# Kernel optimization log

Hardware: AMD Instinct MI355X
Metric: run time of the kernel (lower is better)

Reference implementation:

```python
import jax, jax.numpy as jnp
import numpy as np

WS = (5, 8, 8)   # window_size (Wz, Wh, Ww)
SS = (2, 4, 4)   # shift_size  (Sz, Sh, Sw)
EPS = 1e-5


def _rel_pos_index(ws):
    Wz, Wh, Ww = ws
    coords = np.stack(np.meshgrid(np.arange(Wz), np.arange(Wh), np.arange(Ww), indexing='ij'))
    cf = coords.reshape(3, -1)                      # (3, N)
    rel = cf[:, :, None] - cf[:, None, :]           # (3, N, N)
    rel = rel.transpose(1, 2, 0).astype(np.int64)   # (N, N, 3)
    rel[..., 0] += Wz - 1
    rel[..., 1] += Wh - 1
    rel[..., 2] += Ww - 1
    rel[..., 0] *= (2 * Wh - 1) * (2 * Ww - 1)
    rel[..., 1] *= (2 * Ww - 1)
    return rel.sum(-1)                              # (N, N)


def _shift_mask(Z, H, W, ws, ss):
    Wz, Wh, Ww = ws
    Sz, Sh, Sw = ss
    img = np.zeros((Z, H, W), dtype=np.float32)
    cnt = 0
    for zs in (slice(0, -Wz), slice(-Wz, -Sz), slice(-Sz, None)):
        for hs in (slice(0, -Wh), slice(-Wh, -Sh), slice(-Sh, None)):
            for wl in (slice(0, -Ww), slice(-Ww, -Sw), slice(-Sw, None)):
                img[zs, hs, wl] = cnt
                cnt += 1
    mw = img.reshape(Z // Wz, Wz, H // Wh, Wh, W // Ww, Ww)
    mw = mw.transpose(0, 2, 4, 1, 3, 5).reshape(-1, Wz * Wh * Ww)  # (nW, N)
    diff = mw[:, None, :] - mw[:, :, None]                          # (nW, N, N)
    return np.where(diff != 0, np.float32(-100.0), np.float32(0.0))


def _layernorm(x, g, b):
    mu = jnp.mean(x, axis=-1, keepdims=True)
    var = jnp.var(x, axis=-1, keepdims=True)
    return (x - mu) * jax.lax.rsqrt(var + EPS) * g + b


def setup_inputs() -> dict:
    key = jax.random.key(0)
    ks = jax.random.split(key, 6)
    B, C, Z, H, W = 2, 192, 10, 48, 48
    nH = 6
    hidden = 4 * C
    tbl = (2 * WS[0] - 1) * (2 * WS[1] - 1) * (2 * WS[2] - 1)
    return {
        'x': jax.random.normal(ks[0], (B, C, Z, H, W), jnp.float32),
        'norm1_g': jnp.ones((C,), jnp.float32),
        'norm1_b': jnp.zeros((C,), jnp.float32),
        'qkv_w': jax.random.normal(ks[1], (3 * C, C), jnp.float32) * 0.02,
        'qkv_b': jnp.zeros((3 * C,), jnp.float32),
        'proj_w': jax.random.normal(ks[2], (C, C), jnp.float32) * 0.02,
        'proj_b': jnp.zeros((C,), jnp.float32),
        'rpb_table': jax.random.normal(ks[3], (tbl, nH), jnp.float32) * 0.02,
        'norm2_g': jnp.ones((C,), jnp.float32),
        'norm2_b': jnp.zeros((C,), jnp.float32),
        'fc1_w': jax.random.normal(ks[4], (hidden, C), jnp.float32) * 0.02,
        'fc1_b': jnp.zeros((hidden,), jnp.float32),
        'fc2_w': jax.random.normal(ks[5], (C, hidden), jnp.float32) * 0.02,
        'fc2_b': jnp.zeros((C,), jnp.float32),
    }


def reference(x, norm1_g, norm1_b, qkv_w, qkv_b, proj_w, proj_b, rpb_table,
              norm2_g, norm2_b, fc1_w, fc1_b, fc2_w, fc2_b):
    B, C, Z, H, W = x.shape
    Wz, Wh, Ww = WS
    Sz, Sh, Sw = SS
    nH = rpb_table.shape[1]
    hd = C // nH
    N = Wz * Wh * Ww
    scale = hd ** -0.5

    h = jnp.transpose(x, (0, 2, 3, 4, 1))            # (B,Z,H,W,C) channels-last
    shortcut = h
    h = _layernorm(h, norm1_g, norm1_b)
    # cyclic shift
    h = jnp.roll(h, shift=(-Sz, -Sh, -Sw), axis=(1, 2, 3))
    # window partition -> (BW, N, C)
    win = h.reshape(B, Z // Wz, Wz, H // Wh, Wh, W // Ww, Ww, C)
    win = win.transpose(0, 1, 3, 5, 2, 4, 6, 7).reshape(-1, N, C)
    BW = win.shape[0]

    qkv = win @ qkv_w.T + qkv_b                      # (BW, N, 3C)
    qkv = qkv.reshape(BW, N, 3, nH, hd)
    q = jnp.transpose(qkv[:, :, 0], (0, 2, 1, 3)) * scale   # (BW,nH,N,hd)
    k = jnp.transpose(qkv[:, :, 1], (0, 2, 1, 3))
    v = jnp.transpose(qkv[:, :, 2], (0, 2, 1, 3))

    attn = jnp.einsum('bhnd,bhmd->bhnm', q, k)       # (BW,nH,N,N)
    idx = _rel_pos_index(WS)                          # static (N,N)
    bias = rpb_table[idx.reshape(-1)].reshape(N, N, nH)
    attn = attn + jnp.transpose(bias, (2, 0, 1))[None]

    mask = jnp.asarray(_shift_mask(Z, H, W, WS, SS)) # (nW,N,N), static
    nW = mask.shape[0]
    attn = attn.reshape(B, nW, nH, N, N) + mask[None, :, None]
    attn = jax.nn.softmax(attn.reshape(BW, nH, N, N), axis=-1)

    out = jnp.einsum('bhnm,bhmd->bhnd', attn, v)     # (BW,nH,N,hd)
    out = jnp.transpose(out, (0, 2, 1, 3)).reshape(BW, N, C)
    out = out @ proj_w.T + proj_b

    # window reverse -> (B,Z,H,W,C)
    out = out.reshape(B, Z // Wz, H // Wh, W // Ww, Wz, Wh, Ww, C)
    out = out.transpose(0, 1, 4, 2, 5, 3, 6, 7).reshape(B, Z, H, W, C)
    out = jnp.roll(out, shift=(Sz, Sh, Sw), axis=(1, 2, 3))

    h = shortcut + out
    h2 = _layernorm(h, norm2_g, norm2_b)
    h2 = jax.nn.gelu(h2 @ fc1_w.T + fc1_b, approximate=False)
    h2 = h2 @ fc2_w.T + fc2_b
    h = h + h2
    return jnp.transpose(h, (0, 4, 1, 2, 3))          # back to (B,C,Z,H,W)
```

## Files before the change

### kernel.cpp

```cpp
#include <hip/hip_runtime.h>
#include <hip/hip_bf16.h>

typedef __hip_bfloat16 bf16;
typedef __attribute__((ext_vector_type(4))) float f32x4;
typedef __attribute__((ext_vector_type(8))) short bf16x8;
typedef __attribute__((ext_vector_type(4))) short bf16x4;
typedef __attribute__((ext_vector_type(4))) int i32x4;

#define DEVINL __device__ __forceinline__

constexpr int SPB = 23040;
constexpr int TOK = 46080;
constexpr int NWT = 320;
constexpr int NHEAD = 6;
constexpr int HD = 32;
constexpr int HID = 768;
constexpr int TBL = 2025;
constexpr float SCALE = 0.17677669529663687f;

DEVINL float b2f(bf16 v) { return __bfloat162float(v); }
DEVINL float bflo(unsigned u) { unsigned w = u << 16; return __builtin_bit_cast(float, w); }

DEVINL unsigned cvtpk(float a, float b) {
  unsigned r;
  asm("v_cvt_pk_bf16_f32 %0, %1, %2" : "=v"(r) : "v"(a), "v"(b));
  return r;
}

DEVINL f32x4 mfma16(bf16x4 a, bf16x4 b, f32x4 c) {
#if __has_builtin(__builtin_amdgcn_mfma_f32_16x16x16bf16_1k)
  return __builtin_amdgcn_mfma_f32_16x16x16bf16_1k(a, b, c, 0, 0, 0);
#elif __has_builtin(__builtin_amdgcn_mfma_f32_16x16x16_bf16)
  return __builtin_amdgcn_mfma_f32_16x16x16_bf16(a, b, c, 0, 0, 0);
#else
  f32x4 d;
  asm volatile("v_mfma_f32_16x16x16_bf16 %0, %1, %2, %3\n\ts_nop 7\n\ts_nop 7"
               : "=v"(d) : "v"(a), "v"(b), "v"(c));
  return d;
#endif
}

DEVINL void gload16(const bf16* g, bf16* l) {
  __builtin_amdgcn_global_load_lds(
      (const __attribute__((address_space(1))) void*)g,
      (__attribute__((address_space(3))) void*)l, 16, 0, 0);
}

__global__ void k_flag(const unsigned* __restrict__ g1, int* __restrict__ flag) {
  if (threadIdx.x == 0) flag[0] = (g1[0] == 0x3F800000u) ? 1 : 0;
}

struct CvtArgs {
  const void* src[13];
  bf16* dst[13];
  int n[13];
};

__global__ __launch_bounds__(256) void k_cvt(CvtArgs a, const int* __restrict__ flag) {
  int bi = blockIdx.y;
  int n = a.n[bi];
  bool f32m = flag[0] != 0;
  const float* sf = (const float*)a.src[bi];
  const bf16* sh = (const bf16*)a.src[bi];
  bf16* d = a.dst[bi];
  if (f32m) {
    for (int i = blockIdx.x * 256 + threadIdx.x; i < n; i += gridDim.x * 256)
      d[i] = __float2bfloat16(sf[i]);
  } else {
    for (int i = blockIdx.x * 256 + threadIdx.x; i < n; i += gridDim.x * 256)
      d[i] = sh[i];
  }
}

__global__ __launch_bounds__(256) void k_ln1win(
    const void* __restrict__ xv, const bf16* __restrict__ g, const bf16* __restrict__ be,
    const int* __restrict__ flag, float* __restrict__ hbuf, bf16* __restrict__ win) {
  __shared__ float tile[192][64];
  __shared__ float red[2][4][64];
  __shared__ float stat[2][64];
  int t = threadIdx.x;
  int p = t & 63, q = t >> 6;
  int base = blockIdx.x * 64;
  int b = base / SPB, s0 = base % SPB;
  bool f32m = flag[0] != 0;
  float sum = 0.f, sq = 0.f;
  if (f32m) {
    const float* x = (const float*)xv;
    for (int c = q; c < 192; c += 4) {
      float v = x[(long)(b * 192 + c) * SPB + s0 + p];
      tile[c][p] = v; sum += v; sq += v * v;
    }
  } else {
    const bf16* x = (const bf16*)xv;
    for (int c = q; c < 192; c += 4) {
      float v = b2f(x[(long)(b * 192 + c) * SPB + s0 + p]);
      tile[c][p] = v; sum += v; sq += v * v;
    }
  }
  red[0][q][p] = sum; red[1][q][p] = sq;
  __syncthreads();
  if (t < 64) {
    float s1 = red[0][0][t] + red[0][1][t] + red[0][2][t] + red[0][3][t];
    float s2 = red[1][0][t] + red[1][1][t] + red[1][2][t] + red[1][3][t];
    float mu = s1 * (1.f / 192.f);
    float var = s2 * (1.f / 192.f) - mu * mu;
    stat[0][t] = mu;
    stat[1][t] = rsqrtf(var + 1e-5f);
  }
  __syncthreads();
  int p2 = t >> 2, quad = t & 3;
  int spos = s0 + p2;
  int z = spos / 2304, rm = spos % 2304;
  int hh = rm / 48, ww = rm % 48;
  int zr = z - 2; if (zr < 0) zr += 10;
  int hr = hh - 4; if (hr < 0) hr += 48;
  int wr = ww - 4; if (wr < 0) wr += 48;
  int zw = zr / 5, zi = zr - zw * 5;
  int hw = hr >> 3, hi = hr & 7;
  int wv = wr >> 3, wi = wr & 7;
  int wb = ((b * 2 + zw) * 6 + hw) * 6 + wv;
  int n = (zi * 8 + hi) * 8 + wi;
  float mu = stat[0][p2], rs = stat[1][p2];
  long hb = (long)(b * SPB + spos) * 192;
  long wbse = (long)(wb * NWT + n) * 192;
  for (int c = quad * 48; c < quad * 48 + 48; ++c) {
    float v = tile[c][p2];
    hbuf[hb + c] = v;
    win[wbse + c] = __float2bfloat16((v - mu) * rs * b2f(g[c]) + b2f(be[c]));
  }
}

template <int EPI, int NN>
__global__ __launch_bounds__(256, 5) void k_gemm(
    const bf16* __restrict__ A, const bf16* __restrict__ Wt, const bf16* __restrict__ bias,
    int K, bf16* __restrict__ out0, float* __restrict__ hbuf, void* __restrict__ outb,
    const int* __restrict__ flag) {
  __shared__ __align__(16) char smem[24576];
  bf16* As = (bf16*)smem;
  bf16* Bs = (bf16*)(smem + 16384);

  int t = threadIdx.x;
  constexpr int NBLK = 360 * NN;
  int wg = (blockIdx.x & 7) * (NBLK / 8) + (blockIdx.x >> 3);
  int m0 = (wg / NN) * 128, n0 = (wg % NN) * 64;
  int wave = t >> 6, lane = t & 63;
  int lr = lane & 15, lg = lane >> 4;
  int wbase = t & ~63;
  f32x4 acc[2][4];
#pragma unroll
  for (int a = 0; a < 2; ++a)
#pragma unroll
    for (int bb2 = 0; bb2 < 4; ++bb2) acc[a][bb2] = (f32x4){0.f, 0.f, 0.f, 0.f};

  for (int kc = 0; kc < K; kc += 64) {
#pragma unroll
    for (int it = 0; it < 4; ++it) {
      int s = it * 256 + t;
      int r = s >> 3, c = s & 7;
      int cg = c ^ (r & 7);
      gload16(&A[(long)(m0 + r) * K + kc + cg * 8], As + (it * 256 + wbase) * 8);
    }
#pragma unroll
    for (int it = 0; it < 2; ++it) {
      int s = it * 256 + t;
      int r = s >> 3, c = s & 7;
      int cg = c ^ (r & 7);
      gload16(&Wt[(long)(n0 + r) * K + kc + cg * 8], Bs + (it * 256 + wbase) * 8);
    }
    __syncthreads();
#pragma unroll
    for (int ks = 0; ks < 2; ++ks) {
      int ra = wave * 32 + lr;
      bf16x8 a0 = *(const bf16x8*)(As + ra * 64 + (((ks * 4 + lg) ^ (ra & 7)) * 8));
      bf16x8 a1 = *(const bf16x8*)(As + (ra + 16) * 64 + (((ks * 4 + lg) ^ ((ra + 16) & 7)) * 8));
#pragma unroll
      for (int nn = 0; nn < 4; ++nn) {
        int rb = nn * 16 + lr;
        bf16x8 bfr = *(const bf16x8*)(Bs + rb * 64 + (((ks * 4 + lg) ^ (rb & 7)) * 8));
        acc[0][nn] = __builtin_amdgcn_mfma_f32_16x16x32_bf16(a0, bfr, acc[0][nn], 0, 0, 0);
        acc[1][nn] = __builtin_amdgcn_mfma_f32_16x16x32_bf16(a1, bfr, acc[1][nn], 0, 0, 0);
      }
    }
    __syncthreads();
  }

  if constexpr (EPI == 0) {
    bf16* Ct = (bf16*)smem;
#pragma unroll
    for (int nn = 0; nn < 4; ++nn) {
      int f = n0 + nn * 16 + lr;
      float bv = b2f(bias[f]);
      float sc = (f < 192) ? SCALE : 1.f;
#pragma unroll
      for (int mi = 0; mi < 2; ++mi)
#pragma unroll
        for (int r = 0; r < 4; ++r) {
          int rl = wave * 32 + mi * 16 + lg * 4 + r;
          Ct[rl * 72 + nn * 16 + lr] = __float2bfloat16((acc[mi][nn][r] + bv) * sc);
        }
    }
    __syncthreads();
#pragma unroll
    for (int it = 0; it < 4; ++it) {
      int fi = it * 256 + t;
      int row = fi >> 3, c8 = (fi & 7) * 8;
      int f0 = n0 + c8;
      int plane = f0 >> 5, d0 = f0 & 31;
      long dst = ((long)plane * TOK + m0 + row) * 32 + d0;
      *(i32x4*)&out0[dst] = *(const i32x4*)&Ct[row * 72 + c8];
    }
  } else if constexpr (EPI == 1) {
    float* Cf = (float*)smem;
#pragma unroll
    for (int half = 0; half < 2; ++half) {
      if ((wave >> 1) == half) {
#pragma unroll
        for (int nn = 0; nn < 4; ++nn) {
          int c = n0 + nn * 16 + lr;
          float bv = b2f(bias[c]);
#pragma unroll
          for (int mi = 0; mi < 2; ++mi)
#pragma unroll
            for (int r = 0; r < 4; ++r) {
              int rl = wave * 32 + mi * 16 + lg * 4 + r - half * 64;
              Cf[rl * 68 + nn * 16 + lr] = acc[mi][nn][r] + bv;
            }
        }
      }
      __syncthreads();
#pragma unroll
      for (int it = 0; it < 4; ++it) {
        int fi = it * 256 + t;
        int row = fi >> 4, c4 = (fi & 15) * 4;
        int grow = m0 + half * 64 + row;
        int wb = grow / NWT, i = grow % NWT;
        int b = wb / 72, wIdx = wb % 72;
        int zw = wIdx / 36, hw = (wIdx % 36) / 6, wv = wIdx % 6;
        int zi = i >> 6, hi = (i >> 3) & 7, wi = i & 7;
        int zf = zw * 5 + zi + 2; if (zf >= 10) zf -= 10;
        int hf = hw * 8 + hi + 4; if (hf >= 48) hf -= 48;
        int wf = wv * 8 + wi + 4; if (wf >= 48) wf -= 48;
        long hb = (long)(b * SPB + zf * 2304 + hf * 48 + wf) * 192 + n0 + c4;
        f32x4 cur = *(f32x4*)&hbuf[hb];
        cur += *(const f32x4*)&Cf[row * 68 + c4];
        *(f32x4*)&hbuf[hb] = cur;
      }
      __syncthreads();
    }
  } else if constexpr (EPI == 2) {
    bf16* Ct = (bf16*)smem;
#pragma unroll
    for (int nn = 0; nn < 4; ++nn) {
      int f = n0 + nn * 16 + lr;
      float bv = b2f(bias[f]);
#pragma unroll
      for (int mi = 0; mi < 2; ++mi)
#pragma unroll
        for (int r = 0; r < 4; ++r) {
          int rl = wave * 32 + mi * 16 + lg * 4 + r;
          float v = acc[mi][nn][r] + bv;
          v = 0.5f * v * (1.f + erff(v * 0.70710678118654752f));
          Ct[rl * 72 + nn * 16 + lr] = __float2bfloat16(v);
        }
    }
    __syncthreads();
#pragma unroll
    for (int it = 0; it < 4; ++it) {
      int fi = it * 256 + t;
      int row = fi >> 3, c8 = (fi & 7) * 8;
      long dst = (long)(m0 + row) * HID + n0 + c8;
      *(i32x4*)&out0[dst] = *(const i32x4*)&Ct[row * 72 + c8];
    }
  } else {
    float* eld = (float*)smem;
    int b = m0 / SPB, sbase = m0 % SPB;
    bool f32m = flag[0] != 0;
#pragma unroll
    for (int half = 0; half < 2; ++half) {
      if ((wave >> 1) == half) {
#pragma unroll
        for (int nn = 0; nn < 4; ++nn) {
          int c = n0 + nn * 16 + lr;
          float bv = b2f(bias[c]);
#pragma unroll
          for (int mi = 0; mi < 2; ++mi)
#pragma unroll
            for (int r = 0; r < 4; ++r) {
              int rl = wave * 32 + mi * 16 + lg * 4 + r;
              int row = m0 + rl;
              float v = acc[mi][nn][r] + bv + hbuf[(long)row * 192 + c];
              eld[(rl - half * 64) * 65 + nn * 16 + lr] = v;
            }
        }
      }
      __syncthreads();
      int cl = t >> 2, sq = t & 3;
      long ob = (long)(b * 192 + n0 + cl) * SPB + sbase + half * 64;
      if (f32m) {
        float* ob32 = (float*)outb;
#pragma unroll
        for (int k2 = 0; k2 < 16; ++k2) {
          int sl = sq * 16 + k2;
          ob32[ob + sl] = eld[sl * 65 + cl];
        }
      } else {
        bf16* ob16 = (bf16*)outb;
#pragma unroll
        for (int k2 = 0; k2 < 16; ++k2) {
          int sl = sq * 16 + k2;
          ob16[ob + sl] = __float2bfloat16(eld[sl * 65 + cl]);
        }
      }
      __syncthreads();
    }
  }
}

__global__ __launch_bounds__(256) void k_attn_mfma(
    const bf16* __restrict__ qkv, const bf16* __restrict__ rpb, bf16* __restrict__ o) {
  __shared__ __align__(16) bf16 KlA[320 * 32];
  __shared__ __align__(16) bf16 Vt[32][328];
  __shared__ unsigned short bias_l[2032];
  __shared__ unsigned short info[320];

  int t = threadIdx.x;
  int blk = blockIdx.x;
  int head = blk % NHEAD, wb = blk / NHEAD;
  const bf16* qp = qkv + ((long)head * TOK + wb * NWT) * HD;
  const bf16* kp = qkv + ((long)(6 + head) * TOK + wb * NWT) * HD;
  const bf16* vp = qkv + ((long)(12 + head) * TOK + wb * NWT) * HD;
  int wIdx = wb % 72;
  int wz = wIdx / 36, hw = (wIdx % 36) / 6, wv = wIdx % 6;
  int wbase = t & ~63;

#pragma unroll
  for (int it = 0; it < 5; ++it) {
    int s = it * 256 + t;
    int row = s >> 2, c = s & 3;
    int cg = c ^ (row & 3);
    gload16(&kp[row * 32 + cg * 8], KlA + (it * 256 + wbase) * 8);
  }
#pragma unroll
  for (int it = 0; it < 3; ++it) {
    int idx = t + 256 * it;
    if (idx < 640) {
      int kp2 = idx % 160, c8 = idx / 160;
      i32x4 va = *(const i32x4*)&vp[(kp2 * 2) * HD + c8 * 8];
      i32x4 vb = *(const i32x4*)&vp[(kp2 * 2 + 1) * HD + c8 * 8];
#pragma unroll
      for (int e = 0; e < 8; ++e) {
        unsigned lo = ((unsigned)va[e >> 1] >> ((e & 1) * 16)) & 0xffffu;
        unsigned hi = ((unsigned)vb[e >> 1] >> ((e & 1) * 16)) & 0xffffu;
        *(unsigned*)&Vt[c8 * 8 + e][kp2 * 2] = lo | (hi << 16);
      }
    }
  }
  for (int idx = t; idx < TBL; idx += 256)
    bias_l[idx] = ((const unsigned short*)rpb)[idx * NHEAD + head];
  for (int idx = t; idx < NWT; idx += 256) {
    int zi = idx >> 6, hi2 = (idx >> 3) & 7, wi = idx & 7;
    int zr = wz * 5 + zi, hr = hw * 8 + hi2, wr = wv * 8 + wi;
    int rid = (zr < 5 ? 0 : (zr < 8 ? 9 : 18)) + (hr < 40 ? 0 : (hr < 44 ? 3 : 6)) +
              (wr < 40 ? 0 : (wr < 44 ? 1 : 2));
    info[idx] = (unsigned short)(((zi * 225 + hi2 * 15 + wi) << 5) | rid);
  }
  __syncthreads();

  int wave = t >> 6, lane = t & 63;
  int lr = lane & 15, lg = lane >> 4;
  int csw = (lg ^ (lr & 3)) * 8;

  for (int qi = 0; qi < 5; ++qi) {
    int qbl = qi * 64 + wave * 16;
    bf16x8 qf = *(const bf16x8*)&qp[(qbl + lr) * HD + lg * 8];
    unsigned ciq = info[qbl + lr];
    int ci1012 = (int)(ciq >> 5) + 1012;

    float mph0, sph0, mph1, sph1;
    f32x4 oa00, oa01, oa10, oa11;

#pragma unroll
    for (int ph = 0; ph < 2; ++ph) {
      f32x4 sc[10];
#pragma unroll
      for (int u = 0; u < 10; ++u) {
        int tt = ph * 10 + u;
        bf16x8 kf = *(const bf16x8*)(KlA + (tt * 16 + lr) * 32 + csw);
        sc[u] = __builtin_amdgcn_mfma_f32_16x16x32_bf16(kf, qf, (f32x4){0.f, 0.f, 0.f, 0.f}, 0, 0, 0);
      }
      float mxv = -1e30f;
#pragma unroll
      for (int u = 0; u < 10; ++u) {
        int tt = ph * 10 + u;
        int k0 = tt * 16 + lg * 4;
        unsigned w0 = *(const unsigned*)&info[k0];
        unsigned w1 = *(const unsigned*)&info[k0 + 2];
        unsigned kin0 = w0 & 0xffffu, kin1 = w0 >> 16;
        unsigned kin2 = w1 & 0xffffu, kin3 = w1 >> 16;
        float s0 = sc[u][0] + bflo((unsigned)bias_l[ci1012 - (int)(kin0 >> 5)]);
        float s1 = sc[u][1] + bflo((unsigned)bias_l[ci1012 - (int)(kin1 >> 5)]);
        float s2 = sc[u][2] + bflo((unsigned)bias_l[ci1012 - (int)(kin2 >> 5)]);
        float s3 = sc[u][3] + bflo((unsigned)bias_l[ci1012 - (int)(kin3 >> 5)]);
        if ((kin0 ^ ciq) & 31u) s0 -= 100.f;
        if ((kin1 ^ ciq) & 31u) s1 -= 100.f;
        if ((kin2 ^ ciq) & 31u) s2 -= 100.f;
        if ((kin3 ^ ciq) & 31u) s3 -= 100.f;
        sc[u][0] = s0; sc[u][1] = s1; sc[u][2] = s2; sc[u][3] = s3;
        mxv = fmaxf(mxv, fmaxf(fmaxf(s0, s1), fmaxf(s2, s3)));
      }
      mxv = fmaxf(mxv, __shfl_xor(mxv, 16));
      mxv = fmaxf(mxv, __shfl_xor(mxv, 32));
      float sum = 0.f;
#pragma unroll
      for (int u = 0; u < 10; ++u) {
        float p0 = __expf(sc[u][0] - mxv);
        float p1 = __expf(sc[u][1] - mxv);
        float p2 = __expf(sc[u][2] - mxv);
        float p3 = __expf(sc[u][3] - mxv);
        sc[u][0] = p0; sc[u][1] = p1; sc[u][2] = p2; sc[u][3] = p3;
        sum += (p0 + p1) + (p2 + p3);
      }
      sum += __shfl_xor(sum, 16);
      sum += __shfl_xor(sum, 32);

      f32x4 o0 = {0.f, 0.f, 0.f, 0.f}, o1 = {0.f, 0.f, 0.f, 0.f};
#pragma unroll
      for (int u = 0; u < 10; ++u) {
        int tt = ph * 10 + u;
        unsigned pk0 = cvtpk(sc[u][0], sc[u][1]);
        unsigned pk1 = cvtpk(sc[u][2], sc[u][3]);
        union { unsigned uu[2]; bf16x4 v; } pu;
        pu.uu[0] = pk0; pu.uu[1] = pk1;
        bf16x4 v0 = *(const bf16x4*)&Vt[lr][tt * 16 + lg * 4];
        bf16x4 v1 = *(const bf16x4*)&Vt[16 + lr][tt * 16 + lg * 4];
        o0 = mfma16(pu.v, v0, o0);
        o1 = mfma16(pu.v, v1, o1);
      }
      if (ph == 0) { mph0 = mxv; sph0 = sum; oa00 = o0; oa01 = o1; }
      else         { mph1 = mxv; sph1 = sum; oa10 = o0; oa11 = o1; }
    }

    float m = fmaxf(mph0, mph1);
    float f0 = __expf(mph0 - m), f1 = __expf(mph1 - m);
    float rl = 1.f / (sph0 * f0 + sph1 * f1);
    float a0 = f0 * rl, a1 = f1 * rl;
    int a0i = __builtin_bit_cast(int, a0);
    int a1i = __builtin_bit_cast(int, a1);
#pragma unroll
    for (int r = 0; r < 4; ++r) {
      float s0 = __builtin_bit_cast(float, __builtin_amdgcn_ds_bpermute((lg * 4 + r) * 4, a0i));
      float s1 = __builtin_bit_cast(float, __builtin_amdgcn_ds_bpermute((lg * 4 + r) * 4, a1i));
      bf16* pr = o + ((long)(wb * NWT) + qbl + lg * 4 + r) * 192 + head * 32;
      pr[lr] = __float2bfloat16(oa00[r] * s0 + oa10[r] * s1);
      pr[16 + lr] = __float2bfloat16(oa01[r] * s0 + oa11[r] * s1);
    }
  }
}

__global__ __launch_bounds__(256) void k_ln2(
    const float* __restrict__ h, const bf16* __restrict__ g, const bf16* __restrict__ be,
    bf16* __restrict__ o) {
  int wave = threadIdx.x >> 6, lane = threadIdx.x & 63;
  float g0 = b2f(g[lane]), g1 = b2f(g[lane + 64]), g2 = b2f(g[lane + 128]);
  float b0 = b2f(be[lane]), b1 = b2f(be[lane + 64]), b2v = b2f(be[lane + 128]);
  for (long row = (long)blockIdx.x * 4 + wave; row < TOK; row += (long)gridDim.x * 4) {
    const float* hr = h + row * 192;
    float v0 = hr[lane], v1 = hr[lane + 64], v2 = hr[lane + 128];
    float s1 = v0 + v1 + v2;
    float s2 = v0 * v0 + v1 * v1 + v2 * v2;
#pragma unroll
    for (int off = 32; off > 0; off >>= 1) {
      s1 += __shfl_down(s1, off);
      s2 += __shfl_down(s2, off);
    }
    s1 = __shfl(s1, 0);
    s2 = __shfl(s2, 0);
    float mu = s1 * (1.f / 192.f);
    float rs = rsqrtf(s2 * (1.f / 192.f) - mu * mu + 1e-5f);
    bf16* orow = o + row * 192;
    orow[lane] = __float2bfloat16((v0 - mu) * rs * g0 + b0);
    orow[lane + 64] = __float2bfloat16((v1 - mu) * rs * g1 + b1);
    orow[lane + 128] = __float2bfloat16((v2 - mu) * rs * g2 + b2v);
  }
}

extern "C" void kernel_launch(void* const* d_in, const int* in_sizes, int n_in,
                              void* d_out, int out_size, void* d_ws, size_t ws_size,
                              hipStream_t stream) {
  (void)in_sizes; (void)n_in; (void)out_size; (void)ws_size;

  char* pp = (char*)d_ws;
  float* hbuf = (float*)pp;        pp += (size_t)TOK * 192 * 4;
  bf16* qkv   = (bf16*)pp;         pp += (size_t)3 * TOK * 192 * 2;
  bf16* win   = (bf16*)pp;         pp += (size_t)TOK * 192 * 2;
  bf16* fc1o  = (bf16*)pp;         pp += (size_t)TOK * HID * 2;
  int*  flag  = (int*)pp;          pp += 64;

  const int din_idx[13] = {1, 2, 3, 4, 5, 6, 7, 8, 9, 10, 11, 12, 13};
  const int sizes[13]   = {192, 192, 110592, 576, 36864, 192, 12150, 192, 192,
                           147456, 768, 147456, 192};
  bf16* canon[13];
  for (int ii = 0; ii < 13; ++ii) {
    canon[ii] = (bf16*)pp;
    size_t bytes = ((size_t)sizes[ii] * 2 + 63) & ~(size_t)63;
    pp += bytes;
  }
  bf16* n1g  = canon[0];
  bf16* n1b  = canon[1];
  bf16* qkvw = canon[2];
  bf16* qkvb = canon[3];
  bf16* projw= canon[4];
  bf16* projb= canon[5];
  bf16* rpb  = canon[6];
  bf16* n2g  = canon[7];
  bf16* n2b  = canon[8];
  bf16* fc1w = canon[9];
  bf16* fc1b = canon[10];
  bf16* fc2w = canon[11];
  bf16* fc2b = canon[12];

  CvtArgs ca;
  for (int ii = 0; ii < 13; ++ii) {
    ca.src[ii] = d_in[din_idx[ii]];
    ca.dst[ii] = canon[ii];
    ca.n[ii] = sizes[ii];
  }

  k_flag<<<1, 64, 0, stream>>>((const unsigned*)d_in[1], flag);
  k_cvt<<<dim3(64, 13), 256, 0, stream>>>(ca, flag);
  k_ln1win<<<TOK / 64, 256, 0, stream>>>(d_in[0], n1g, n1b, flag, hbuf, win);
  k_gemm<0, 9><<<360 * 9, 256, 0, stream>>>(win, qkvw, qkvb, 192, qkv, nullptr, nullptr, flag);
  k_attn_mfma<<<864, 256, 0, stream>>>(qkv, rpb, win);
  k_gemm<1, 3><<<360 * 3, 256, 0, stream>>>(win, projw, projb, 192, nullptr, hbuf, nullptr, flag);
  k_ln2<<<2048, 256, 0, stream>>>(hbuf, n2g, n2b, win);
  k_gemm<2, 12><<<360 * 12, 256, 0, stream>>>(win, fc1w, fc1b, 192, fc1o, nullptr, nullptr, flag);
  k_gemm<3, 3><<<360 * 3, 256, 0, stream>>>(fc1o, fc2w, fc2b, 768, nullptr, hbuf, d_out, flag);
}
```

Baseline: 235.8 us.

## Fuse projection GEMM, residual add and LayerNorm2 into one kernel

Replaces the proj GEMM (3 column tiles per row block) plus the separate LN2 kernel with a single kernel where each block computes all 192 output columns for 128 rows. It then adds the residual into hbuf and computes the LayerNorm in registers via lane shuffles, writing bf16 output into the reused qkv buffer. This removes one launch and a full re-read of hbuf, but the grid drops to 360 blocks and the epilogue does scattered per-element global stores with 24 accumulators per thread.

```diff
diff --git a/kernel.cpp b/kernel.cpp
--- a/kernel.cpp
+++ b/kernel.cpp
@@ -209,44 +209,6 @@
       long dst = ((long)plane * TOK + m0 + row) * 32 + d0;
       *(i32x4*)&out0[dst] = *(const i32x4*)&Ct[row * 72 + c8];
     }
-  } else if constexpr (EPI == 1) {
-    float* Cf = (float*)smem;
-#pragma unroll
-    for (int half = 0; half < 2; ++half) {
-      if ((wave >> 1) == half) {
-#pragma unroll
-        for (int nn = 0; nn < 4; ++nn) {
-          int c = n0 + nn * 16 + lr;
-          float bv = b2f(bias[c]);
-#pragma unroll
-          for (int mi = 0; mi < 2; ++mi)
-#pragma unroll
-            for (int r = 0; r < 4; ++r) {
-              int rl = wave * 32 + mi * 16 + lg * 4 + r - half * 64;
-              Cf[rl * 68 + nn * 16 + lr] = acc[mi][nn][r] + bv;
-            }
-        }
-      }
-      __syncthreads();
-#pragma unroll
-      for (int it = 0; it < 4; ++it) {
-        int fi = it * 256 + t;
-        int row = fi >> 4, c4 = (fi & 15) * 4;
-        int grow = m0 + half * 64 + row;
-        int wb = grow / NWT, i = grow % NWT;
-        int b = wb / 72, wIdx = wb % 72;
-        int zw = wIdx / 36, hw = (wIdx % 36) / 6, wv = wIdx % 6;
-        int zi = i >> 6, hi = (i >> 3) & 7, wi = i & 7;
-        int zf = zw * 5 + zi + 2; if (zf >= 10) zf -= 10;
-        int hf = hw * 8 + hi + 4; if (hf >= 48) hf -= 48;
-        int wf = wv * 8 + wi + 4; if (wf >= 48) wf -= 48;
-        long hb = (long)(b * SPB + zf * 2304 + hf * 48 + wf) * 192 + n0 + c4;
-        f32x4 cur = *(f32x4*)&hbuf[hb];
-        cur += *(const f32x4*)&Cf[row * 68 + c4];
-        *(f32x4*)&hbuf[hb] = cur;
-      }
-      __syncthreads();
-    }
   } else if constexpr (EPI == 2) {
     bf16* Ct = (bf16*)smem;
 #pragma unroll
@@ -314,6 +276,97 @@
       __syncthreads();
     }
   }
+}
+
+__global__ __launch_bounds__(256) void k_projln2(
+    const bf16* __restrict__ A, const bf16* __restrict__ Wt, const bf16* __restrict__ bias,
+    const bf16* __restrict__ g2, const bf16* __restrict__ b2,
+    float* __restrict__ hbuf, bf16* __restrict__ lnout) {
+  __shared__ __align__(16) char smem[40960];
+  bf16* As = (bf16*)smem;
+  bf16* Bs = (bf16*)(smem + 16384);
+
+  int t = threadIdx.x;
+  int wg = (blockIdx.x & 7) * 45 + (blockIdx.x >> 3);
+  int m0 = wg * 128;
+  int wave = t >> 6, lane = t & 63;
+  int lr = lane & 15, lg = lane >> 4;
+  int wbase = t & ~63;
+  f32x4 acc[2][12];
+#pragma unroll
+  for (int a = 0; a < 2; ++a)
+#pragma unroll
+    for (int bb2 = 0; bb2 < 12; ++bb2) acc[a][bb2] = (f32x4){0.f, 0.f, 0.f, 0.f};
+
+  for (int kc = 0; kc < 192; kc += 64) {
+#pragma unroll
+    for (int it = 0; it < 4; ++it) {
+      int s = it * 256 + t;
+      int r = s >> 3, c = s & 7;
+      int cg = c ^ (r & 7);
+      gload16(&A[(long)(m0 + r) * 192 + kc + cg * 8], As + (it * 256 + wbase) * 8);
+    }
+#pragma unroll
+    for (int it = 0; it < 6; ++it) {
+      int s = it * 256 + t;
+      int r = s >> 3, c = s & 7;
+      int cg = c ^ (r & 7);
+      gload16(&Wt[(long)r * 192 + kc + cg * 8], Bs + (it * 256 + wbase) * 8);
+    }
+    __syncthreads();
+#pragma unroll
+    for (int ks = 0; ks < 2; ++ks) {
+      int ra = wave * 32 + lr;
+      bf16x8 a0 = *(const bf16x8*)(As + ra * 64 + (((ks * 4 + lg) ^ (ra & 7)) * 8));
+      bf16x8 a1 = *(const bf16x8*)(As + (ra + 16) * 64 + (((ks * 4 + lg) ^ ((ra + 16) & 7)) * 8));
+#pragma unroll
+      for (int nn = 0; nn < 12; ++nn) {
+        int rb = nn * 16 + lr;
+        bf16x8 bfr = *(const bf16x8*)(Bs + rb * 64 + (((ks * 4 + lg) ^ (rb & 7)) * 8));
+        acc[0][nn] = __builtin_amdgcn_mfma_f32_16x16x32_bf16(a0, bfr, acc[0][nn], 0, 0, 0);
+        acc[1][nn] = __builtin_amdgcn_mfma_f32_16x16x32_bf16(a1, bfr, acc[1][nn], 0, 0, 0);
+      }
+    }
+    __syncthreads();
+  }
+
+#pragma unroll
+  for (int mi = 0; mi < 2; ++mi)
+#pragma unroll
+    for (int r = 0; r < 4; ++r) {
+      int grow = m0 + wave * 32 + mi * 16 + lg * 4 + r;
+      int wb = grow / NWT, i = grow % NWT;
+      int b = wb / 72, wIdx = wb % 72;
+      int zw = wIdx / 36, hw = (wIdx % 36) / 6, wv = wIdx % 6;
+      int zi = i >> 6, hi = (i >> 3) & 7, wi = i & 7;
+      int zf = zw * 5 + zi + 2; if (zf >= 10) zf -= 10;
+      int hf = hw * 8 + hi + 4; if (hf >= 48) hf -= 48;
+      int wf = wv * 8 + wi + 4; if (wf >= 48) wf -= 48;
+      long s = (long)(b * SPB + zf * 2304 + hf * 48 + wf);
+      float v[12];
+      float sum = 0.f, sq = 0.f;
+#pragma unroll
+      for (int nn = 0; nn < 12; ++nn) {
+        int c = nn * 16 + lr;
+        float x = acc[mi][nn][r] + b2f(bias[c]) + hbuf[s * 192 + c];
+        v[nn] = x;
+        hbuf[s * 192 + c] = x;
+        sum += x;
+        sq += x * x;
+      }
+#pragma unroll
+      for (int off = 1; off < 16; off <<= 1) {
+        sum += __shfl_xor(sum, off);
+        sq += __shfl_xor(sq, off);
+      }
+      float mu = sum * (1.f / 192.f);
+      float rs = rsqrtf(sq * (1.f / 192.f) - mu * mu + 1e-5f);
+#pragma unroll
+      for (int nn = 0; nn < 12; ++nn) {
+        int c = nn * 16 + lr;
+        lnout[s * 192 + c] = __float2bfloat16((v[nn] - mu) * rs * b2f(g2[c]) + b2f(b2[c]));
+      }
+    }
 }
 
 __global__ __launch_bounds__(256) void k_attn_mfma(
@@ -457,33 +510,6 @@
   }
 }
 
-__global__ __launch_bounds__(256) void k_ln2(
-    const float* __restrict__ h, const bf16* __restrict__ g, const bf16* __restrict__ be,
-    bf16* __restrict__ o) {
-  int wave = threadIdx.x >> 6, lane = threadIdx.x & 63;
-  float g0 = b2f(g[lane]), g1 = b2f(g[lane + 64]), g2 = b2f(g[lane + 128]);
-  float b0 = b2f(be[lane]), b1 = b2f(be[lane + 64]), b2v = b2f(be[lane + 128]);
-  for (long row = (long)blockIdx.x * 4 + wave; row < TOK; row += (long)gridDim.x * 4) {
-    const float* hr = h + row * 192;
-    float v0 = hr[lane], v1 = hr[lane + 64], v2 = hr[lane + 128];
-    float s1 = v0 + v1 + v2;
-    float s2 = v0 * v0 + v1 * v1 + v2 * v2;
-#pragma unroll
-    for (int off = 32; off > 0; off >>= 1) {
-      s1 += __shfl_down(s1, off);
-      s2 += __shfl_down(s2, off);
-    }
-    s1 = __shfl(s1, 0);
-    s2 = __shfl(s2, 0);
-    float mu = s1 * (1.f / 192.f);
-    float rs = rsqrtf(s2 * (1.f / 192.f) - mu * mu + 1e-5f);
-    bf16* orow = o + row * 192;
-    orow[lane] = __float2bfloat16((v0 - mu) * rs * g0 + b0);
-    orow[lane + 64] = __float2bfloat16((v1 - mu) * rs * g1 + b1);
-    orow[lane + 128] = __float2bfloat16((v2 - mu) * rs * g2 + b2v);
-  }
-}
-
 extern "C" void kernel_launch(void* const* d_in, const int* in_sizes, int n_in,
                               void* d_out, int out_size, void* d_ws, size_t ws_size,
                               hipStream_t stream) {
@@ -495,6 +521,8 @@
   bf16* win   = (bf16*)pp;         pp += (size_t)TOK * 192 * 2;
   bf16* fc1o  = (bf16*)pp;         pp += (size_t)TOK * HID * 2;
   int*  flag  = (int*)pp;          pp += 64;
+
+  bf16* ln2o = qkv;
 
   const int din_idx[13] = {1, 2, 3, 4, 5, 6, 7, 8, 9, 10, 11, 12, 13};
   const int sizes[13]   = {192, 192, 110592, 576, 36864, 192, 12150, 192, 192,
@@ -531,8 +559,7 @@
   k_ln1win<<<TOK / 64, 256, 0, stream>>>(d_in[0], n1g, n1b, flag, hbuf, win);
   k_gemm<0, 9><<<360 * 9, 256, 0, stream>>>(win, qkvw, qkvb, 192, qkv, nullptr, nullptr, flag);
   k_attn_mfma<<<864, 256, 0, stream>>>(qkv, rpb, win);
-  k_gemm<1, 3><<<360 * 3, 256, 0, stream>>>(win, projw, projb, 192, nullptr, hbuf, nullptr, flag);
-  k_ln2<<<2048, 256, 0, stream>>>(hbuf, n2g, n2b, win);
-  k_gemm<2, 12><<<360 * 12, 256, 0, stream>>>(win, fc1w, fc1b, 192, fc1o, nullptr, nullptr, flag);
+  k_projln2<<<360, 256, 0, stream>>>(win, projw, projb, n2g, n2b, hbuf, ln2o);
+  k_gemm<2, 12><<<360 * 12, 256, 0, stream>>>(ln2o, fc1w, fc1b, 192, fc1o, nullptr, nullptr, flag);
   k_gemm<3, 3><<<360 * 3, 256, 0, stream>>>(fc1o, fc2w, fc2b, 768, nullptr, hbuf, d_out, flag);
 }
```

Result: slower. 243.6 us (+3.3%).
